# Performance work log

Measured on AMD Instinct MI355X. Metric: run time of the kernel, lower is better.

Reference implementation:

```python
import jax, jax.numpy as jnp
import numpy as np

D = 1024      # model_dim
H = 16        # num_attention_heads
HD = D // H   # head dim
FFN = 4096    # ffn_dim
EPS = 1e-5


def _mha(q_in, k_in, v_in, wq, bq, wk, bk, wv, bv):
    B, Sq, _ = q_in.shape
    Sk = k_in.shape[1]
    def split(x, S):
        return x.reshape(B, S, H, HD).transpose(0, 2, 1, 3)  # [B,H,S,HD]
    Q = split(q_in @ wq + bq, Sq)
    K = split(k_in @ wk + bk, Sk)
    V = split(v_in @ wv + bv, Sk)
    scores = jnp.einsum('bhqd,bhkd->bhqk', Q, K) / (HD ** 0.5)
    probs = jax.nn.softmax(scores, axis=-1)
    ctx = jnp.einsum('bhqk,bhkd->bhqd', probs, V)
    return ctx.transpose(0, 2, 1, 3).reshape(B, Sq, D)


def _ln(x, g, b):
    mu = jnp.mean(x, axis=-1, keepdims=True)
    var = jnp.mean(jnp.square(x - mu), axis=-1, keepdims=True)
    return (x - mu) * jax.lax.rsqrt(var + EPS) * g + b


def setup_inputs() -> dict:
    key = jax.random.key(0)
    ks = jax.random.split(key, 24)
    s = 1.0 / np.sqrt(D)
    inp = {
        'hidden_states': jax.random.normal(ks[0], (2, 2048, D), jnp.float32),
        'encoder_hidden_states': jax.random.normal(ks[1], (2, 2048, D), jnp.float32),
        # self-attention projections
        'sa_wq': jax.random.normal(ks[2], (D, D), jnp.float32) * s,
        'sa_bq': jnp.zeros((D,), jnp.float32),
        'sa_wk': jax.random.normal(ks[3], (D, D), jnp.float32) * s,
        'sa_bk': jnp.zeros((D,), jnp.float32),
        'sa_wv': jax.random.normal(ks[4], (D, D), jnp.float32) * s,
        'sa_bv': jnp.zeros((D,), jnp.float32),
        'ln1_g': jnp.ones((D,), jnp.float32),
        'ln1_b': jnp.zeros((D,), jnp.float32),
        # cross-attention projections
        'ca_wq': jax.random.normal(ks[5], (D, D), jnp.float32) * s,
        'ca_bq': jnp.zeros((D,), jnp.float32),
        'ca_wk': jax.random.normal(ks[6], (D, D), jnp.float32) * s,
        'ca_bk': jnp.zeros((D,), jnp.float32),
        'ca_wv': jax.random.normal(ks[7], (D, D), jnp.float32) * s,
        'ca_bv': jnp.zeros((D,), jnp.float32),
        'ln2_g': jnp.ones((D,), jnp.float32),
        'ln2_b': jnp.zeros((D,), jnp.float32),
        # feed-forward
        'fc1_w': jax.random.normal(ks[8], (D, FFN), jnp.float32) * s,
        'fc1_b': jnp.zeros((FFN,), jnp.float32),
        'fc2_w': jax.random.normal(ks[9], (FFN, D), jnp.float32) * (1.0 / np.sqrt(FFN)),
        'fc2_b': jnp.zeros((D,), jnp.float32),
        'ln3_g': jnp.ones((D,), jnp.float32),
        'ln3_b': jnp.zeros((D,), jnp.float32),
    }
    return inp


def reference(hidden_states, encoder_hidden_states,
              sa_wq, sa_bq, sa_wk, sa_bk, sa_wv, sa_bv, ln1_g, ln1_b,
              ca_wq, ca_bq, ca_wk, ca_bk, ca_wv, ca_bv, ln2_g, ln2_b,
              fc1_w, fc1_b, fc2_w, fc2_b, ln3_g, ln3_b):
    # self-attention + residual + LN  (dropout = identity in eval)
    h = _mha(hidden_states, hidden_states, hidden_states,
             sa_wq, sa_bq, sa_wk, sa_bk, sa_wv, sa_bv)
    x = _ln(hidden_states + h, ln1_g, ln1_b)
    # cross-attention + residual + LN
    h = _mha(x, encoder_hidden_states, encoder_hidden_states,
             ca_wq, ca_bq, ca_wk, ca_bk, ca_wv, ca_bv)
    x = _ln(x + h, ln2_g, ln2_b)
    # feed-forward + residual + LN
    h = jax.nn.relu(x @ fc1_w + fc1_b) @ fc2_w + fc2_b
    return _ln(x + h, ln3_g, ln3_b)
```

## Files before the change

### kernel.cpp

```cpp
#include <hip/hip_runtime.h>


typedef unsigned short u16;
typedef unsigned int u32;
typedef short v8s __attribute__((ext_vector_type(8)));
typedef float v4f __attribute__((ext_vector_type(4)));

#define LDP 72
#define LOG2E 1.44269504088896340736f

__device__ __forceinline__ float b2f(u16 h) {
    return __uint_as_float(((u32)h) << 16);
}
__device__ __forceinline__ u16 f2b(float f) {
    u32 u = __float_as_uint(f);
    u += 0x7fffu + ((u >> 16) & 1u);
    return (u16)(u >> 16);
}
__device__ __forceinline__ u32 pack2_rz(float lo, float hi) {
    return (__float_as_uint(hi) & 0xffff0000u) | (__float_as_uint(lo) >> 16);
}
__device__ __forceinline__ void gload16(const void* g, void* l) {
    __builtin_amdgcn_global_load_lds(
        (const __attribute__((address_space(1))) unsigned int*)g,
        (__attribute__((address_space(3))) unsigned int*)l, 16, 0, 0);
}
__device__ __forceinline__ int xcd_swz(int orig, int nwg) {
    const int q = nwg >> 3, r = nwg & 7;
    const int xcd = orig & 7, idx = orig >> 3;
    return (xcd < r ? xcd * (q + 1) : r * (q + 1) + (xcd - r) * q) + idx;
}

__global__ __launch_bounds__(256) void conv_f2b(
    const float* __restrict__ src, u16* __restrict__ dst)
{
    const size_t i = ((size_t)blockIdx.x * 256 + threadIdx.x) * 8;
    float4 a = *(const float4*)&src[i];
    float4 b = *(const float4*)&src[i + 4];
    ushort4 o0, o1;
    o0.x = f2b(a.x); o0.y = f2b(a.y); o0.z = f2b(a.z); o0.w = f2b(a.w);
    o1.x = f2b(b.x); o1.y = f2b(b.y); o1.z = f2b(b.z); o1.w = f2b(b.w);
    *(ushort4*)&dst[i] = o0;
    *(ushort4*)&dst[i + 4] = o1;
}

__global__ __launch_bounds__(256) void transpose_f2b(
    const float* __restrict__ src, u16* __restrict__ dst, int R, int C)
{
    __shared__ u16 tile[32][33];
    const int t  = threadIdx.x;
    const int tx = t & 31, ty = t >> 5;
    const int r0 = blockIdx.y * 32, c0 = blockIdx.x * 32;
#pragma unroll
    for (int i = 0; i < 32; i += 8)
        tile[ty + i][tx] = f2b(src[(size_t)(r0 + ty + i) * C + c0 + tx]);
    __syncthreads();
#pragma unroll
    for (int i = 0; i < 32; i += 8)
        dst[(size_t)(c0 + ty + i) * R + r0 + tx] = tile[tx][ty + i];
}

__global__ __launch_bounds__(256) void prep_bias(
    const float* __restrict__ bq, const float* __restrict__ bk, const float* __restrict__ bv,
    const float* __restrict__ cbk, const float* __restrict__ cbv,
    float* __restrict__ sab, float* __restrict__ cakvb)
{
    int i = blockIdx.x * 256 + threadIdx.x;
    if (i < 1024) {
        sab[i]          = bq[i];
        sab[1024 + i]   = bk[i];
        sab[2048 + i]   = bv[i];
        cakvb[i]        = cbk[i];
        cakvb[1024 + i] = cbv[i];
    }
}

template <int BN>
__global__ __launch_bounds__(256) void gemm_bt(
    const u16* __restrict__ A, const u16* __restrict__ Bt,
    const float* __restrict__ bias, u16* __restrict__ C,
    int M, int N, int K, int relu, int qcols, float qscale,
    u16* __restrict__ vt, int vtcol0)
{
    constexpr int NI = BN / 32;
    __shared__ __align__(16) u16 Al[128 * 64];
    __shared__ __align__(16) u16 Bl[BN * 64];
    const int tid  = threadIdx.x;
    const int wave = tid >> 6, lane = tid & 63;
    const int quad = lane >> 4, tl = lane & 15;
    const int nwg  = gridDim.x * gridDim.y;
    const int wgid = xcd_swz(blockIdx.y * gridDim.x + blockIdx.x, nwg);
    const int bx   = wgid % gridDim.x, by = wgid / gridDim.x;
    const int bm0 = by * 128, bn0 = bx * BN;
    const int wm = (wave >> 1) * 64, wn = (wave & 1) * (BN / 2);
    const int srow = lane >> 3;
    const int scol = (((lane & 7) ^ srow) << 3);

    const v4f z4 = {0.f, 0.f, 0.f, 0.f};
    v4f acc[4][NI];
#pragma unroll
    for (int i = 0; i < 4; ++i)
#pragma unroll
        for (int j = 0; j < NI; ++j) acc[i][j] = z4;

    for (int kt = 0; kt < K; kt += 64) {
#pragma unroll
        for (int i = 0; i < 4; ++i) {
            const int c = wave * 4 + i;
            const int row = c * 8 + srow;
            gload16(&A[(size_t)(bm0 + row) * K + kt + scol], &Al[c * 512]);
        }
#pragma unroll
        for (int i = 0; i < NI; ++i) {
            const int c = wave * NI + i;
            const int row = c * 8 + srow;
            gload16(&Bt[(size_t)(bn0 + row) * K + kt + scol], &Bl[c * 512]);
        }
        __syncthreads();
#pragma unroll
        for (int kk = 0; kk < 2; ++kk) {
            const int pc = ((kk * 4 + quad) ^ (tl & 7)) << 3;
            v8s af[4], bf[NI];
#pragma unroll
            for (int i = 0; i < 4; ++i) af[i] = *(const v8s*)&Al[(wm + i * 16 + tl) * 64 + pc];
#pragma unroll
            for (int i = 0; i < NI; ++i) bf[i] = *(const v8s*)&Bl[(wn + i * 16 + tl) * 64 + pc];
#pragma unroll
            for (int mi = 0; mi < 4; ++mi)
#pragma unroll
                for (int ni = 0; ni < NI; ++ni)
                    acc[mi][ni] = __builtin_amdgcn_mfma_f32_16x16x32_bf16(
                        af[mi], bf[ni], acc[mi][ni], 0, 0, 0);
        }
        __syncthreads();
    }
#pragma unroll
    for (int ni = 0; ni < NI; ++ni) {
        int col = bn0 + wn + ni * 16 + tl;
        float bv = bias[col];
        if (vtcol0 >= 0 && col >= vtcol0) {
            int cv = col - vtcol0;
            int h = cv >> 6, hd = cv & 63;
#pragma unroll
            for (int mi = 0; mi < 4; ++mi) {
                int row0 = bm0 + wm + mi * 16 + (quad << 2);
                int bb = row0 >> 11, s = row0 & 2047;
                ushort4 pk;
                pk.x = f2b(acc[mi][ni][0] + bv);
                pk.y = f2b(acc[mi][ni][1] + bv);
                pk.z = f2b(acc[mi][ni][2] + bv);
                pk.w = f2b(acc[mi][ni][3] + bv);
                *(ushort4*)&vt[((size_t)(bb * 16 + h) * 64 + hd) * 2048 + s] = pk;
            }
        } else {
            float sc = (col < qcols) ? qscale : 1.0f;
#pragma unroll
            for (int mi = 0; mi < 4; ++mi) {
                int row0 = bm0 + wm + mi * 16 + (quad << 2);
#pragma unroll
                for (int r = 0; r < 4; ++r) {
                    float vv = acc[mi][ni][r] + bv;
                    if (relu) vv = fmaxf(vv, 0.f);
                    vv *= sc;
                    C[(size_t)(row0 + r) * N + col] = f2b(vv);
                }
            }
        }
    }
}

__global__ __launch_bounds__(256) void attn_v6(
    const u16* __restrict__ Q, int qs, const u16* __restrict__ Kp, int ks,
    const u16* __restrict__ Vt, u16* __restrict__ O, int os, int Sk)
{
    __shared__ __align__(16) u16 Kl[128 * 64];
    __shared__ __align__(16) u16 Vtl[64 * 128];
    __shared__ __align__(16) u16 Pl[4][32 * LDP];

    const int tid  = threadIdx.x;
    const int wave = tid >> 6, lane = tid & 63;
    const int quad = lane >> 4, tl = lane & 15;
    const int nwg  = gridDim.x * gridDim.y;
    const int wgid = xcd_swz(blockIdx.y * gridDim.x + blockIdx.x, nwg);
    const int bx   = wgid % gridDim.x, by = wgid / gridDim.x;
    const int b = by >> 4, h = by & 15;
    const int srow = lane >> 3;
    const int scolK = (((lane & 7) ^ srow) << 3);
    const int vri = lane >> 4, vj = lane & 15;

    const u16* qb  = Q  + (size_t)(b * 2048) * qs + h * 64;
    const u16* kb  = Kp + (size_t)(b * 2048) * ks + h * 64;
    const u16* vtb = Vt + (size_t)by * 64 * 2048;
    u16*       ob  = O  + (size_t)(b * 2048) * os + h * 64;
    const int qr0 = bx * 128 + wave * 32;

    v8s qf[2][2];
#pragma unroll
    for (int mi = 0; mi < 2; ++mi)
#pragma unroll
        for (int kk = 0; kk < 2; ++kk)
            qf[mi][kk] = *(const v8s*)&qb[(size_t)(qr0 + mi * 16 + tl) * qs + kk * 32 + quad * 8];

    const v4f z4 = {0.f, 0.f, 0.f, 0.f};
    v4f oacc[2][4] = {{z4, z4, z4, z4}, {z4, z4, z4, z4}};
    float l_q[2] = {0.f, 0.f};
    u16* Pw = &Pl[wave][0];

    const int pc0 = (quad ^ (tl & 7)) << 3;
    const int pc1 = ((4 + quad) ^ (tl & 7)) << 3;

    for (int kt = 0; kt < Sk; kt += 128) {
#pragma unroll
        for (int i = 0; i < 4; ++i) {
            const int c = wave * 4 + i;
            const int row = c * 8 + srow;
            gload16(&kb[(size_t)(kt + row) * ks + scolK], &Kl[c * 512]);
        }
#pragma unroll
        for (int i = 0; i < 4; ++i) {
            const int c = wave * 4 + i;
            const int vr = c * 4 + vri;
            const int g = (vj & 8) | ((vj & 7) ^ (vr & 7));
            gload16(&vtb[(size_t)vr * 2048 + kt + (g << 3)], &Vtl[c * 512]);
        }
        __syncthreads();

#pragma unroll
        for (int hf = 0; hf < 2; ++hf) {
#pragma unroll
            for (int nt = 0; nt < 4; ++nt) {
                const int krow = ((hf * 4 + nt) * 16 + tl) * 64;
                v8s k0 = *(const v8s*)&Kl[krow + pc0];
                v8s k1 = *(const v8s*)&Kl[krow + pc1];
#pragma unroll
                for (int mi = 0; mi < 2; ++mi) {
                    v4f a = z4;
                    a = __builtin_amdgcn_mfma_f32_16x16x32_bf16(k0, qf[mi][0], a, 0, 0, 0);
                    a = __builtin_amdgcn_mfma_f32_16x16x32_bf16(k1, qf[mi][1], a, 0, 0, 0);
                    float p0 = exp2f(a[0]), p1 = exp2f(a[1]);
                    float p2 = exp2f(a[2]), p3 = exp2f(a[3]);
                    l_q[mi] += (p0 + p1) + (p2 + p3);
                    uint2 pk;
                    pk.x = pack2_rz(p0, p1);
                    pk.y = pack2_rz(p2, p3);
                    *(uint2*)&Pw[(mi * 16 + tl) * LDP + nt * 16 + quad * 4] = pk;
                }
            }
            asm volatile("" ::: "memory");

            v8s pf[2][2];
#pragma unroll
            for (int mi = 0; mi < 2; ++mi) {
                pf[mi][0] = *(const v8s*)&Pw[(mi * 16 + tl) * LDP + quad * 8];
                pf[mi][1] = *(const v8s*)&Pw[(mi * 16 + tl) * LDP + 32 + quad * 8];
            }
            const int pv0 = ((hf * 8) | (quad ^ (tl & 7))) << 3;
            const int pv1 = ((hf * 8) | ((4 + quad) ^ (tl & 7))) << 3;
            __builtin_amdgcn_s_setprio(1);
#pragma unroll
            for (int d = 0; d < 4; ++d) {
                const int vbase = (d * 16 + tl) * 128;
                v8s v0 = *(const v8s*)&Vtl[vbase + pv0];
                v8s v1 = *(const v8s*)&Vtl[vbase + pv1];
#pragma unroll
                for (int mi = 0; mi < 2; ++mi) {
                    oacc[mi][d] = __builtin_amdgcn_mfma_f32_16x16x32_bf16(pf[mi][0], v0, oacc[mi][d], 0, 0, 0);
                    oacc[mi][d] = __builtin_amdgcn_mfma_f32_16x16x32_bf16(pf[mi][1], v1, oacc[mi][d], 0, 0, 0);
                }
            }
            __builtin_amdgcn_s_setprio(0);
            asm volatile("" ::: "memory");
        }
        __syncthreads();
    }

#pragma unroll
    for (int mi = 0; mi < 2; ++mi) {
        l_q[mi] += __shfl_xor(l_q[mi], 16);
        l_q[mi] += __shfl_xor(l_q[mi], 32);
    }

#pragma unroll
    for (int mi = 0; mi < 2; ++mi)
#pragma unroll
        for (int r = 0; r < 4; ++r) {
            float inv = 1.0f / __shfl(l_q[mi], quad * 4 + r);
#pragma unroll
            for (int d = 0; d < 4; ++d)
                ob[(size_t)(qr0 + mi * 16 + quad * 4 + r) * os + d * 16 + tl] =
                    f2b(oacc[mi][d][r] * inv);
        }
}

template <int XF32, int OF32>
__global__ __launch_bounds__(256) void add_ln(
    const void* __restrict__ Xv, const u16* __restrict__ Hh,
    const float* __restrict__ G, const float* __restrict__ Bb,
    void* __restrict__ Outv)
{
    const int row = blockIdx.x, t = threadIdx.x;
    float v0, v1, v2, v3;
    {
        ushort4 hv = *(const ushort4*)&Hh[(size_t)row * 1024 + t * 4];
        if (XF32) {
            const float* xr = (const float*)Xv + (size_t)row * 1024;
            float4 xv = *(const float4*)&xr[t * 4];
            v0 = xv.x + b2f(hv.x); v1 = xv.y + b2f(hv.y);
            v2 = xv.z + b2f(hv.z); v3 = xv.w + b2f(hv.w);
        } else {
            const u16* xr = (const u16*)Xv + (size_t)row * 1024;
            ushort4 xv = *(const ushort4*)&xr[t * 4];
            v0 = b2f(xv.x) + b2f(hv.x); v1 = b2f(xv.y) + b2f(hv.y);
            v2 = b2f(xv.z) + b2f(hv.z); v3 = b2f(xv.w) + b2f(hv.w);
        }
    }

    float s1 = v0 + v1 + v2 + v3;
    float s2 = v0 * v0 + v1 * v1 + v2 * v2 + v3 * v3;
#pragma unroll
    for (int o = 1; o < 64; o <<= 1) {
        s1 += __shfl_xor(s1, o);
        s2 += __shfl_xor(s2, o);
    }
    __shared__ float red[8];
    const int wave = t >> 6, lane = t & 63;
    if (lane == 0) { red[wave] = s1; red[4 + wave] = s2; }
    __syncthreads();
    s1 = red[0] + red[1] + red[2] + red[3];
    s2 = red[4] + red[5] + red[6] + red[7];

    const float mu = s1 * (1.f / 1024.f);
    float var = s2 * (1.f / 1024.f) - mu * mu;
    var = fmaxf(var, 0.f);
    const float rs = rsqrtf(var + 1e-5f);

    float4 gv = *(const float4*)&G[t * 4];
    float4 bv = *(const float4*)&Bb[t * 4];
    float o0 = (v0 - mu) * rs * gv.x + bv.x;
    float o1 = (v1 - mu) * rs * gv.y + bv.y;
    float o2 = (v2 - mu) * rs * gv.z + bv.z;
    float o3 = (v3 - mu) * rs * gv.w + bv.w;

    if (OF32) {
        float4 ov = {o0, o1, o2, o3};
        *(float4*)&((float*)Outv)[(size_t)row * 1024 + t * 4] = ov;
    } else {
        ushort4 ov;
        ov.x = f2b(o0); ov.y = f2b(o1); ov.z = f2b(o2); ov.w = f2b(o3);
        *(ushort4*)&((u16*)Outv)[(size_t)row * 1024 + t * 4] = ov;
    }
}

extern "C" void kernel_launch(void* const* d_in, const int* in_sizes, int n_in,
                              void* d_out, int out_size, void* d_ws, size_t ws_size,
                              hipStream_t stream) {
    const float* x0  = (const float*)d_in[0];
    const float* enc = (const float*)d_in[1];

    char* wsb = (char*)d_ws;
    const size_t MB = 1024u * 1024u;
    u16*   wt_sa   = (u16*)(wsb);
    u16*   wt_caq  = (u16*)(wsb + 6  * MB);
    u16*   wt_cakv = (u16*)(wsb + 8  * MB);
    float* sab     = (float*)(wsb + 12 * MB);
    float* cakvb   = (float*)(wsb + 12 * MB + 16384);
    char*  arena   = wsb + 12 * MB + 32768;
    u16* QKV    = (u16*)(arena);
    u16* hbuf   = (u16*)(arena + 24 * MB);
    u16* x0b    = (u16*)(arena + 24 * MB);
    u16* encb   = (u16*)(arena + 24 * MB);
    u16* x1     = (u16*)(arena + 32 * MB);
    u16* Vt     = (u16*)(arena + 40 * MB);
    u16* Q2     = (u16*)(arena);
    u16* KV2    = (u16*)(arena + 8  * MB);
    u16* x2     = (u16*)(arena);
    u16* wt_fc1 = (u16*)(wsb);
    u16* wt_fc2 = (u16*)(arena + 8  * MB);
    u16* tbuf   = (u16*)(arena + 16 * MB);
    u16* h3     = (u16*)(wsb);

    const float QSC = 0.125f * LOG2E;

    prep_bias<<<4, 256, 0, stream>>>(
        (const float*)d_in[3], (const float*)d_in[5], (const float*)d_in[7],
        (const float*)d_in[13], (const float*)d_in[15], sab, cakvb);

    transpose_f2b<<<dim3(32, 32), 256, 0, stream>>>((const float*)d_in[2],  wt_sa,               1024, 1024);
    transpose_f2b<<<dim3(32, 32), 256, 0, stream>>>((const float*)d_in[4],  wt_sa + 1024*1024,   1024, 1024);
    transpose_f2b<<<dim3(32, 32), 256, 0, stream>>>((const float*)d_in[6],  wt_sa + 2*1024*1024, 1024, 1024);
    transpose_f2b<<<dim3(32, 32), 256, 0, stream>>>((const float*)d_in[10], wt_caq,              1024, 1024);
    transpose_f2b<<<dim3(32, 32), 256, 0, stream>>>((const float*)d_in[12], wt_cakv,             1024, 1024);
    transpose_f2b<<<dim3(32, 32), 256, 0, stream>>>((const float*)d_in[14], wt_cakv + 1024*1024, 1024, 1024);

    conv_f2b<<<2048, 256, 0, stream>>>(x0, x0b);
    gemm_bt<128><<<dim3(24, 32), 256, 0, stream>>>(
        x0b, wt_sa, sab, QKV, 4096, 3072, 1024, 0, 1024, QSC, Vt, 2048);
    attn_v6<<<dim3(16, 32), 256, 0, stream>>>(QKV, 3072, QKV + 1024, 3072, Vt, hbuf, 1024, 2048);
    add_ln<1, 0><<<4096, 256, 0, stream>>>(x0, hbuf, (const float*)d_in[8], (const float*)d_in[9], x1);

    conv_f2b<<<2048, 256, 0, stream>>>(enc, encb);
    gemm_bt<64><<<dim3(16, 32), 256, 0, stream>>>(
        x1, wt_caq, (const float*)d_in[11], Q2, 4096, 1024, 1024, 0, 1024, QSC, (u16*)nullptr, -1);
    gemm_bt<128><<<dim3(16, 32), 256, 0, stream>>>(
        encb, wt_cakv, cakvb, KV2, 4096, 2048, 1024, 0, 0, 1.0f, Vt, 1024);
    attn_v6<<<dim3(16, 32), 256, 0, stream>>>(Q2, 1024, KV2, 2048, Vt, hbuf, 1024, 2048);
    add_ln<0, 0><<<4096, 256, 0, stream>>>(x1, hbuf, (const float*)d_in[16], (const float*)d_in[17], x2);

    transpose_f2b<<<dim3(128, 32), 256, 0, stream>>>((const float*)d_in[18], wt_fc1, 1024, 4096);
    transpose_f2b<<<dim3(32, 128), 256, 0, stream>>>((const float*)d_in[20], wt_fc2, 4096, 1024);
    gemm_bt<128><<<dim3(32, 32), 256, 0, stream>>>(
        x2, wt_fc1, (const float*)d_in[19], tbuf, 4096, 4096, 1024, 1, 0, 1.0f, (u16*)nullptr, -1);
    gemm_bt<64><<<dim3(16, 32), 256, 0, stream>>>(
        tbuf, wt_fc2, (const float*)d_in[21], h3, 4096, 1024, 4096, 0, 0, 1.0f, (u16*)nullptr, -1);
    add_ln<0, 1><<<4096, 256, 0, stream>>>(x2, h3, (const float*)d_in[22], (const float*)d_in[23], d_out);
}
```

Baseline: 522.2 us.

## Split attention work across 8 waves with 16 query rows each

The attention kernel now launches 512 threads per block (8 waves), and each wave handles 16 query rows instead of 32. K/V tile loads are spread over twice as many waves, and per-wave accumulators and P buffers are halved. The aim is more waves in flight to hide LDS and exp latency, and lower register pressure. In exchange, each K/V LDS fragment is reused by only one query tile per wave, so LDS read traffic per FLOP doubles.

```diff
diff --git a/kernel.cpp b/kernel.cpp
--- a/kernel.cpp
+++ b/kernel.cpp
@@ -169,13 +169,13 @@
     }
 }
 
-__global__ __launch_bounds__(256) void attn_v6(
+__global__ __launch_bounds__(512) void attn_v7(
     const u16* __restrict__ Q, int qs, const u16* __restrict__ Kp, int ks,
     const u16* __restrict__ Vt, u16* __restrict__ O, int os, int Sk)
 {
     __shared__ __align__(16) u16 Kl[128 * 64];
     __shared__ __align__(16) u16 Vtl[64 * 128];
-    __shared__ __align__(16) u16 Pl[4][32 * LDP];
+    __shared__ __align__(16) u16 Pl[8][16 * LDP];
 
     const int tid  = threadIdx.x;
     const int wave = tid >> 6, lane = tid & 63;
@@ -192,18 +192,16 @@
     const u16* kb  = Kp + (size_t)(b * 2048) * ks + h * 64;
     const u16* vtb = Vt + (size_t)by * 64 * 2048;
     u16*       ob  = O  + (size_t)(b * 2048) * os + h * 64;
-    const int qr0 = bx * 128 + wave * 32;
-
-    v8s qf[2][2];
-#pragma unroll
-    for (int mi = 0; mi < 2; ++mi)
-#pragma unroll
-        for (int kk = 0; kk < 2; ++kk)
-            qf[mi][kk] = *(const v8s*)&qb[(size_t)(qr0 + mi * 16 + tl) * qs + kk * 32 + quad * 8];
+    const int qr0 = bx * 128 + wave * 16;
+
+    v8s qf[2];
+#pragma unroll
+    for (int kk = 0; kk < 2; ++kk)
+        qf[kk] = *(const v8s*)&qb[(size_t)(qr0 + tl) * qs + kk * 32 + quad * 8];
 
     const v4f z4 = {0.f, 0.f, 0.f, 0.f};
-    v4f oacc[2][4] = {{z4, z4, z4, z4}, {z4, z4, z4, z4}};
-    float l_q[2] = {0.f, 0.f};
+    v4f oacc[4] = {z4, z4, z4, z4};
+    float l_q = 0.f;
     u16* Pw = &Pl[wave][0];
 
     const int pc0 = (quad ^ (tl & 7)) << 3;
@@ -211,14 +209,14 @@
 
     for (int kt = 0; kt < Sk; kt += 128) {
 #pragma unroll
-        for (int i = 0; i < 4; ++i) {
-            const int c = wave * 4 + i;
+        for (int i = 0; i < 2; ++i) {
+            const int c = wave * 2 + i;
             const int row = c * 8 + srow;
             gload16(&kb[(size_t)(kt + row) * ks + scolK], &Kl[c * 512]);
         }
 #pragma unroll
-        for (int i = 0; i < 4; ++i) {
-            const int c = wave * 4 + i;
+        for (int i = 0; i < 2; ++i) {
+            const int c = wave * 2 + i;
             const int vr = c * 4 + vri;
             const int g = (vj & 8) | ((vj & 7) ^ (vr & 7));
             gload16(&vtb[(size_t)vr * 2048 + kt + (g << 3)], &Vtl[c * 512]);
@@ -232,28 +230,21 @@
                 const int krow = ((hf * 4 + nt) * 16 + tl) * 64;
                 v8s k0 = *(const v8s*)&Kl[krow + pc0];
                 v8s k1 = *(const v8s*)&Kl[krow + pc1];
-#pragma unroll
-                for (int mi = 0; mi < 2; ++mi) {
-                    v4f a = z4;
-                    a = __builtin_amdgcn_mfma_f32_16x16x32_bf16(k0, qf[mi][0], a, 0, 0, 0);
-                    a = __builtin_amdgcn_mfma_f32_16x16x32_bf16(k1, qf[mi][1], a, 0, 0, 0);
-                    float p0 = exp2f(a[0]), p1 = exp2f(a[1]);
-                    float p2 = exp2f(a[2]), p3 = exp2f(a[3]);
-                    l_q[mi] += (p0 + p1) + (p2 + p3);
-                    uint2 pk;
-                    pk.x = pack2_rz(p0, p1);
-                    pk.y = pack2_rz(p2, p3);
-                    *(uint2*)&Pw[(mi * 16 + tl) * LDP + nt * 16 + quad * 4] = pk;
-                }
+                v4f a = z4;
+                a = __builtin_amdgcn_mfma_f32_16x16x32_bf16(k0, qf[0], a, 0, 0, 0);
+                a = __builtin_amdgcn_mfma_f32_16x16x32_bf16(k1, qf[1], a, 0, 0, 0);
+                float p0 = exp2f(a[0]), p1 = exp2f(a[1]);
+                float p2 = exp2f(a[2]), p3 = exp2f(a[3]);
+                l_q += (p0 + p1) + (p2 + p3);
+                uint2 pk;
+                pk.x = pack2_rz(p0, p1);
+                pk.y = pack2_rz(p2, p3);
+                *(uint2*)&Pw[tl * LDP + nt * 16 + quad * 4] = pk;
             }
             asm volatile("" ::: "memory");
 
-            v8s pf[2][2];
-#pragma unroll
-            for (int mi = 0; mi < 2; ++mi) {
-                pf[mi][0] = *(const v8s*)&Pw[(mi * 16 + tl) * LDP + quad * 8];
-                pf[mi][1] = *(const v8s*)&Pw[(mi * 16 + tl) * LDP + 32 + quad * 8];
-            }
+            v8s pf0 = *(const v8s*)&Pw[tl * LDP + quad * 8];
+            v8s pf1 = *(const v8s*)&Pw[tl * LDP + 32 + quad * 8];
             const int pv0 = ((hf * 8) | (quad ^ (tl & 7))) << 3;
             const int pv1 = ((hf * 8) | ((4 + quad) ^ (tl & 7))) << 3;
             __builtin_amdgcn_s_setprio(1);
@@ -262,11 +253,8 @@
                 const int vbase = (d * 16 + tl) * 128;
                 v8s v0 = *(const v8s*)&Vtl[vbase + pv0];
                 v8s v1 = *(const v8s*)&Vtl[vbase + pv1];
-#pragma unroll
-                for (int mi = 0; mi < 2; ++mi) {
-                    oacc[mi][d] = __builtin_amdgcn_mfma_f32_16x16x32_bf16(pf[mi][0], v0, oacc[mi][d], 0, 0, 0);
-                    oacc[mi][d] = __builtin_amdgcn_mfma_f32_16x16x32_bf16(pf[mi][1], v1, oacc[mi][d], 0, 0, 0);
-                }
+                oacc[d] = __builtin_amdgcn_mfma_f32_16x16x32_bf16(pf0, v0, oacc[d], 0, 0, 0);
+                oacc[d] = __builtin_amdgcn_mfma_f32_16x16x32_bf16(pf1, v1, oacc[d], 0, 0, 0);
             }
             __builtin_amdgcn_s_setprio(0);
             asm volatile("" ::: "memory");
@@ -274,22 +262,17 @@
         __syncthreads();
     }
 
-#pragma unroll
-    for (int mi = 0; mi < 2; ++mi) {
-        l_q[mi] += __shfl_xor(l_q[mi], 16);
-        l_q[mi] += __shfl_xor(l_q[mi], 32);
-    }
-
-#pragma unroll
-    for (int mi = 0; mi < 2; ++mi)
-#pragma unroll
-        for (int r = 0; r < 4; ++r) {
-            float inv = 1.0f / __shfl(l_q[mi], quad * 4 + r);
-#pragma unroll
-            for (int d = 0; d < 4; ++d)
-                ob[(size_t)(qr0 + mi * 16 + quad * 4 + r) * os + d * 16 + tl] =
-                    f2b(oacc[mi][d][r] * inv);
-        }
+    l_q += __shfl_xor(l_q, 16);
+    l_q += __shfl_xor(l_q, 32);
+
+#pragma unroll
+    for (int r = 0; r < 4; ++r) {
+        float inv = 1.0f / __shfl(l_q, quad * 4 + r);
+#pragma unroll
+        for (int d = 0; d < 4; ++d)
+            ob[(size_t)(qr0 + quad * 4 + r) * os + d * 16 + tl] =
+                f2b(oacc[d][r] * inv);
+    }
 }
 
 template <int XF32, int OF32>
@@ -395,7 +378,7 @@
     conv_f2b<<<2048, 256, 0, stream>>>(x0, x0b);
     gemm_bt<128><<<dim3(24, 32), 256, 0, stream>>>(
         x0b, wt_sa, sab, QKV, 4096, 3072, 1024, 0, 1024, QSC, Vt, 2048);
-    attn_v6<<<dim3(16, 32), 256, 0, stream>>>(QKV, 3072, QKV + 1024, 3072, Vt, hbuf, 1024, 2048);
+    attn_v7<<<dim3(16, 32), 512, 0, stream>>>(QKV, 3072, QKV + 1024, 3072, Vt, hbuf, 1024, 2048);
     add_ln<1, 0><<<4096, 256, 0, stream>>>(x0, hbuf, (const float*)d_in[8], (const float*)d_in[9], x1);
 
     conv_f2b<<<2048, 256, 0, stream>>>(enc, encb);
@@ -403,7 +386,7 @@
         x1, wt_caq, (const float*)d_in[11], Q2, 4096, 1024, 1024, 0, 1024, QSC, (u16*)nullptr, -1);
     gemm_bt<128><<<dim3(16, 32), 256, 0, stream>>>(
         encb, wt_cakv, cakvb, KV2, 4096, 2048, 1024, 0, 0, 1.0f, Vt, 1024);
-    attn_v6<<<dim3(16, 32), 256, 0, stream>>>(Q2, 1024, KV2, 2048, Vt, hbuf, 1024, 2048);
+    attn_v7<<<dim3(16, 32), 512, 0, stream>>>(Q2, 1024, KV2, 2048, Vt, hbuf, 1024, 2048);
     add_ln<0, 0><<<4096, 256, 0, stream>>>(x1, hbuf, (const float*)d_in[16], (const float*)d_in[17], x2);
 
     transpose_f2b<<<dim3(128, 32), 256, 0, stream>>>((const float*)d_in[18], wt_fc1, 1024, 4096);
```

Result: no change. 524.7 us (+0.5%).
